# Kernel tuning notes

Hardware: AMD Instinct MI355X
Metric: run time of the kernel (lower is better)

## Reference

```python
import jax, jax.numpy as jnp
import numpy as np
from jax import lax

B, T, D = 16384, 60, 36   # n_traj, n_tp, n_dims
L, C, S = 10, 20, 9       # latent_dim, cluster_num, n_static
OUT = 8                   # mlp out (use_static=False)


def setup_inputs() -> dict:
    key = jax.random.key(0)
    ks = jax.random.split(key, 12)

    def w(k, shape):
        return jax.random.normal(k, shape, jnp.float32) / np.float32(np.sqrt(shape[0]))

    return {
        "data": jax.random.normal(ks[0], (B, T, D), jnp.float32),
        "time_steps": jnp.arange(T, dtype=jnp.float32),
        "static_data": jax.random.normal(ks[1], (B, S), jnp.float32),
        # GRU_unit_cluster gates: Linear(latent_dim + input_dim -> latent_dim)
        "W_update": w(ks[2], (L + D, L)), "b_update": jnp.zeros((L,), jnp.float32),
        "W_reset": w(ks[3], (L + D, L)), "b_reset": jnp.zeros((L,), jnp.float32),
        "W_new": w(ks[4], (L + D, L)), "b_new": jnp.zeros((L,), jnp.float32),
        # infer_emitter_z: Linear(latent_dim + cluster_num -> cluster_num)
        "W_emit": w(ks[5], (L + C, C)), "b_emit": jnp.zeros((C,), jnp.float32),
        # stand-in ODE func (z0_diffeq_solver.ode_func): tanh(Linear(latent->latent))
        "W_ode": w(ks[6], (L, L)), "b_ode": jnp.zeros((L,), jnp.float32),
        # final mlp: Linear(ts*10 + static -> 8)
        "W_mlp": w(ks[7], (T * L + S, OUT)), "b_mlp": jnp.zeros((OUT,), jnp.float32),
    }


def _forward(data, time_steps, static_data,
             W_update, b_update, W_reset, b_reset, W_new, b_new,
             W_emit, b_emit, W_ode, b_ode, W_mlp, b_mlp):
    n_traj = data.shape[0]
    # per-step dt: first step uses the synthetic 0.01 offset, then consecutive diffs
    dts = jnp.concatenate([jnp.full((1,), 0.01, time_steps.dtype), jnp.diff(time_steps)])
    xs = jnp.swapaxes(data, 0, 1)  # [T, B, D]

    def step(carry, inp):
        y_state, y_prob = carry        # [B, L], [B, C]
        x_t, dt = inp                  # [B, D], scalar
        # Euler step of the ODE between observations
        yi_ode = y_state + jnp.tanh(y_state @ W_ode + b_ode) * dt
        # GRU_unit_cluster update
        yc = jnp.concatenate([yi_ode, x_t], axis=-1)          # [B, L+D]
        u = jax.nn.sigmoid(yc @ W_update + b_update)
        r = jax.nn.sigmoid(yc @ W_reset + b_reset)
        cc = jnp.concatenate([yi_ode * r, x_t], axis=-1)
        new = cc @ W_new + b_new
        y_new = (1.0 - u) * new + u * yi_ode                  # [B, L]
        # emit_probs (concat_data=True path)
        zin = jnp.concatenate([y_prob, y_new], axis=-1)       # [B, C+L]
        y_prob_new = jax.nn.softmax(zin @ W_emit + b_emit, axis=-1)
        return (y_new, y_prob_new), y_new

    init = (jnp.zeros((n_traj, L), data.dtype), jnp.zeros((n_traj, C), data.dtype))
    _, states = lax.scan(step, init, (xs, dts))               # states: [T, B, L]

    vec = jnp.swapaxes(states, 0, 1).reshape(n_traj, T * L)   # [B, T*L]
    vec = jnp.concatenate([vec, static_data], axis=-1)        # [B, T*L + S]
    return vec @ W_mlp + b_mlp                                # [B, 8]


def reference(data, time_steps, static_data,
              W_update, b_update, W_reset, b_reset, W_new, b_new,
              W_emit, b_emit, W_ode, b_ode, W_mlp, b_mlp):
    return _forward(data, time_steps, static_data,
                    W_update, b_update, W_reset, b_reset, W_new, b_new,
                    W_emit, b_emit, W_ode, b_ode, W_mlp, b_mlp)
```

## Files before the change

kernel.cpp:

```cpp
#include <hip/hip_runtime.h>
#include <hip/hip_fp16.h>
#include <math.h>

#define B_TRAJ 16384
#define T_STEPS 60
#define D_IN 36
#define L_DIM 10
#define C_NUM 20
#define S_STAT 9
#define OUT_DIM 8
#define TT 2
#define NTILE (T_STEPS / TT)

#define LOG2E 1.4426950408889634f

typedef float f32x2 __attribute__((ext_vector_type(2)));
__device__ __forceinline__ f32x2 pkfma(f32x2 a, f32x2 b, f32x2 c) {
    return __builtin_elementwise_fma(a, b, c);
}

__device__ __forceinline__ float rcp_fast(float x) { return __builtin_amdgcn_rcpf(x); }
__device__ __forceinline__ float exp2_fast(float x) { return __builtin_amdgcn_exp2f(x); }
__device__ __forceinline__ float sigm_fast(float x) {
    return rcp_fast(1.0f + exp2_fast(x * -LOG2E));
}
__device__ __forceinline__ float tanh_fast(float x) {
    const float t = fminf(fmaxf(x * (2.0f * LOG2E), -30.0f), 30.0f);
    return fmaf(-2.0f, rcp_fast(exp2_fast(t) + 1.0f), 1.0f);
}
#define WFENCE() __builtin_amdgcn_wave_barrier()

__global__ __launch_bounds__(256) __attribute__((amdgpu_waves_per_eu(4, 8)))
void dgm2_v7(
    const float* __restrict__ data,
    const float* __restrict__ time_steps,
    const float* __restrict__ static_data,
    const float* __restrict__ W_update,
    const float* __restrict__ b_update,
    const float* __restrict__ W_reset,
    const float* __restrict__ b_reset,
    const float* __restrict__ W_new,
    const float* __restrict__ b_new,
    const float* __restrict__ W_emit,
    const float* __restrict__ b_emit,
    const float* __restrict__ W_ode,
    const float* __restrict__ b_ode,
    const float* __restrict__ W_mlp,
    const float* __restrict__ b_mlp,
    float* __restrict__ out)
{
    __shared__ __align__(16) __half xprojH[8][61][32];
    __shared__ __align__(16) float WGX[D_IN][32];
    __shared__ __align__(16) float wbuf[4][292];
    __shared__ float dts[T_STEPS];

    const int tid  = threadIdx.x;
    const int w    = tid >> 6;
    const int lane = tid & 63;
    const int half = lane >> 5;
    const int s    = lane & 31;
    const int ltraj = w * 2 + half;
    const int traj  = blockIdx.x * 8 + ltraj;

    for (int i = tid; i < D_IN * 30; i += 256) {
        const int k = i / 30, c = i % 30;
        float v;
        if (c < 10)      v = W_update[(L_DIM + k) * L_DIM + c];
        else if (c < 20) v = W_reset [(L_DIM + k) * L_DIM + (c - 10)];
        else             v = W_new   [(L_DIM + k) * L_DIM + (c - 20)];
        WGX[k][c] = v;
    }
    for (int i = tid; i < D_IN * 2; i += 256) WGX[i >> 1][30 + (i & 1)] = 0.0f;
    if (tid < T_STEPS) dts[tid] = (tid == 0) ? 0.01f : time_steps[tid] - time_steps[tid - 1];
    __syncthreads();

    float bcol = 0.0f;
    if (s < 10)      bcol = b_update[s];
    else if (s < 20) bcol = b_reset[s - 10];
    else if (s < 30) bcol = b_new[s - 20];

    {
        f32x2 wxp2[18];
#pragma unroll
        for (int j = 0; j < 18; ++j) wxp2[j] = (f32x2){WGX[2 * j][s], WGX[2 * j + 1][s]};

        float* xst = &wbuf[w][0];
        const float* tbase = data + (size_t)(blockIdx.x * 8 + w * 2) * (T_STEPS * D_IN);
        const int sh  = lane / 18;
        const int sr  = lane % 18;
        const int stt = sr / 9;
        const int sc  = sr % 9;
        const bool stg = (lane < 36);

        if (stg) {
            const float4 v = *reinterpret_cast<const float4*>(
                tbase + (size_t)sh * (T_STEPS * D_IN) + stt * D_IN + sc * 4);
            *reinterpret_cast<float4*>(xst + ((0 * 2 + sh) * TT + stt) * 36 + sc * 4) = v;
        }
        WFENCE();

        for (int tile = 0; tile < NTILE; ++tile) {
            const int cb = tile & 1, nb = cb ^ 1;
            float4 pf = make_float4(0.f, 0.f, 0.f, 0.f);
            if (stg && (tile + 1 < NTILE)) {
                pf = *reinterpret_cast<const float4*>(
                    tbase + (size_t)sh * (T_STEPS * D_IN) + ((tile + 1) * TT + stt) * D_IN + sc * 4);
            }
#pragma unroll
            for (int tt = 0; tt < TT; ++tt) {
                const float* xrow = xst + ((cb * 2 + half) * TT + tt) * 36;
                f32x2 acc2 = (f32x2){bcol, 0.0f};
#pragma unroll
                for (int c = 0; c < 9; ++c) {
                    const float4 x4 = *reinterpret_cast<const float4*>(xrow + c * 4);
                    acc2 = pkfma((f32x2){x4.x, x4.y}, wxp2[2 * c],     acc2);
                    acc2 = pkfma((f32x2){x4.z, x4.w}, wxp2[2 * c + 1], acc2);
                }
                if (s < 30) xprojH[ltraj][tile * TT + tt][s] = __float2half(acc2.x + acc2.y);
            }
            if (stg && (tile + 1 < NTILE)) {
                *reinterpret_cast<float4*>(xst + ((nb * 2 + sh) * TT + stt) * 36 + sc * 4) = pf;
            }
            WFENCE();
        }
    }

    const bool uo = (s < 10);
    const bool ro = (s >= 10 && s < 20);
    const bool no = (s >= 20 && s < 30);
    const bool eo = (s >= 10 && s < 30);
    const int  gcol = uo ? s : (ro ? (s - 10) : (no ? (s - 20) : 0));

    const float* Wg = uo ? W_update : (ro ? W_reset : W_new);
    f32x2 wgy2[5];
#pragma unroll
    for (int j = 0; j < 5; ++j) {
        const float w0 = (s < 30) ? Wg[(2 * j)     * L_DIM + gcol] : 0.0f;
        const float w1 = (s < 30) ? Wg[(2 * j + 1) * L_DIM + gcol] : 0.0f;
        wgy2[j] = (f32x2){w0, w1};
    }

    f32x2 waux2[15];
#pragma unroll
    for (int j = 0; j < 15; ++j) {
        float v0 = 0.0f, v1 = 0.0f;
        if (eo)            { v0 = W_emit[(2 * j) * C_NUM + (s - 10)];
                             v1 = W_emit[(2 * j + 1) * C_NUM + (s - 10)]; }
        else if (uo && j < 5) { v0 = W_ode[(2 * j) * L_DIM + s];
                                v1 = W_ode[(2 * j + 1) * L_DIM + s]; }
        waux2[j] = (f32x2){v0, v1};
    }
    const float bode  = uo ? b_ode[s] : 0.0f;
    const float bemit = eo ? b_emit[s - 10] : 0.0f;

    float* bcYI = &wbuf[w][0]  + half * 12;
    float* bcR  = &wbuf[w][24] + half * 12;
    float* bcN  = &wbuf[w][48] + half * 12;
    float* bcY  = &wbuf[w][72] + half * 12;
    float* bcP  = &wbuf[w][96] + half * 20;

    f32x2 y2[5];
#pragma unroll
    for (int k = 0; k < 5; ++k) y2[k] = (f32x2){0.0f, 0.0f};
    float yown = 0.0f;
    if (eo) bcP[s - 10] = 0.0f;
    WFENCE();

    for (int t = 0; t < T_STEPS; ++t) {
        const float dt = dts[t];

        f32x2 g2 = (f32x2){bode, 0.0f};
#pragma unroll
        for (int k = 0; k < 5; ++k) g2 = pkfma(y2[k], waux2[k], g2);
        const float yis = fmaf(tanh_fast(g2.x + g2.y), dt, yown);
        if (uo) bcYI[s] = yis;
        WFENCE();
        {
            const float4 a = *reinterpret_cast<const float4*>(bcYI);
            const float4 b = *reinterpret_cast<const float4*>(bcYI + 4);
            const float2 c = *reinterpret_cast<const float2*>(bcYI + 8);
            y2[0] = (f32x2){a.x, a.y}; y2[1] = (f32x2){a.z, a.w};
            y2[2] = (f32x2){b.x, b.y}; y2[3] = (f32x2){b.z, b.w};
            y2[4] = (f32x2){c.x, c.y};
        }
        const float yi_r = bcYI[gcol];

        const float xa = __half2float(xprojH[ltraj][t][s]);
        f32x2 ay2 = (f32x2){xa, 0.0f};
#pragma unroll
        for (int k = 0; k < 5; ++k) ay2 = pkfma(y2[k], wgy2[k], ay2);
        const float uval = sigm_fast(ay2.x + ay2.y);
        if (ro) bcR[s - 10] = uval * yi_r;
        WFENCE();

        f32x2 n2 = (f32x2){xa, 0.0f};
        {
            const float4 a = *reinterpret_cast<const float4*>(bcR);
            const float4 b = *reinterpret_cast<const float4*>(bcR + 4);
            const float2 c = *reinterpret_cast<const float2*>(bcR + 8);
            n2 = pkfma((f32x2){a.x, a.y}, wgy2[0], n2);
            n2 = pkfma((f32x2){a.z, a.w}, wgy2[1], n2);
            n2 = pkfma((f32x2){b.x, b.y}, wgy2[2], n2);
            n2 = pkfma((f32x2){b.z, b.w}, wgy2[3], n2);
            n2 = pkfma((f32x2){c.x, c.y}, wgy2[4], n2);
        }
        const float accN = n2.x + n2.y;
        if (no) bcN[s - 20] = accN;
        WFENCE();

        if (uo) {
            const float nv = bcN[s];
            const float yn = fmaf(uval, yis - nv, nv);
            yown = yn;
            bcY[s] = yn;
            xprojH[ltraj][t][s] = __float2half(yn);
        }
        WFENCE();
        {
            const float4 a = *reinterpret_cast<const float4*>(bcY);
            const float4 b = *reinterpret_cast<const float4*>(bcY + 4);
            const float2 c = *reinterpret_cast<const float2*>(bcY + 8);
            y2[0] = (f32x2){a.x, a.y}; y2[1] = (f32x2){a.z, a.w};
            y2[2] = (f32x2){b.x, b.y}; y2[3] = (f32x2){b.z, b.w};
            y2[4] = (f32x2){c.x, c.y};
        }

        f32x2 zd2 = (f32x2){0.0f, 0.0f};
        f32x2 zs2 = (f32x2){0.0f, 0.0f};
#pragma unroll
        for (int q = 0; q < 5; ++q) {
            const float4 z4 = *reinterpret_cast<const float4*>(bcP + q * 4);
            const f32x2 za = (f32x2){z4.x, z4.y};
            const f32x2 zb = (f32x2){z4.z, z4.w};
            zd2 = pkfma(za, waux2[2 * q],     zd2);
            zd2 = pkfma(zb, waux2[2 * q + 1], zd2);
            zs2 = zs2 + za + zb;
        }
        const float zsum = zs2.x + zs2.y;
        const float pinv = (t == 0) ? 0.0f : rcp_fast(zsum);
        f32x2 ev2 = (f32x2){fmaf(zd2.x + zd2.y, pinv, bemit), 0.0f};
#pragma unroll
        for (int k = 0; k < 5; ++k) ev2 = pkfma(y2[k], waux2[10 + k], ev2);
        const float zv = exp2_fast(fminf((ev2.x + ev2.y) * LOG2E, 86.0f));
        if (eo) bcP[s - 10] = zv;
        WFENCE();
    }

    WFENCE();
    {
        const int g = s >> 3, col = s & 7;
        f32x2 o2 = (f32x2){0.0f, 0.0f};
        for (int tb = 0; tb < 15; ++tb) {
            const int t = g + tb * 4;
            const __half2* yh = reinterpret_cast<const __half2*>(&xprojH[ltraj][t][0]);
            const float* wrow = W_mlp + (size_t)t * L_DIM * OUT_DIM + col;
#pragma unroll
            for (int q = 0; q < 5; ++q) {
                const float2 yv = __half22float2(yh[q]);
                const f32x2 w2 = (f32x2){wrow[(2 * q) * OUT_DIM], wrow[(2 * q + 1) * OUT_DIM]};
                o2 = pkfma((f32x2){yv.x, yv.y}, w2, o2);
            }
        }
        float o8 = o2.x + o2.y;
        o8 += __shfl_xor(o8, 8, 32);
        o8 += __shfl_xor(o8, 16, 32);
        if (s < OUT_DIM) {
            const float* stp = static_data + (size_t)traj * S_STAT;
            const float* wms = W_mlp + (size_t)(T_STEPS * L_DIM) * OUT_DIM;
#pragma unroll
            for (int i = 0; i < S_STAT; ++i) o8 += stp[i] * wms[i * OUT_DIM + s];
            out[(size_t)traj * OUT_DIM + s] = o8 + b_mlp[s];
        }
    }
}

extern "C" void kernel_launch(void* const* d_in, const int* in_sizes, int n_in,
                              void* d_out, int out_size, void* d_ws, size_t ws_size,
                              hipStream_t stream) {
    const float* data        = (const float*)d_in[0];
    const float* time_steps  = (const float*)d_in[1];
    const float* static_data = (const float*)d_in[2];
    const float* W_update    = (const float*)d_in[3];
    const float* b_update    = (const float*)d_in[4];
    const float* W_reset     = (const float*)d_in[5];
    const float* b_reset     = (const float*)d_in[6];
    const float* W_new       = (const float*)d_in[7];
    const float* b_new       = (const float*)d_in[8];
    const float* W_emit      = (const float*)d_in[9];
    const float* b_emit      = (const float*)d_in[10];
    const float* W_ode       = (const float*)d_in[11];
    const float* b_ode       = (const float*)d_in[12];
    const float* W_mlp       = (const float*)d_in[13];
    const float* b_mlp       = (const float*)d_in[14];
    float* out = (float*)d_out;

    dim3 grid(B_TRAJ / 8), block(256);
    hipLaunchKernelGGL(dgm2_v7, grid, block, 0, stream,
                       data, time_steps, static_data,
                       W_update, b_update, W_reset, b_reset, W_new, b_new,
                       W_emit, b_emit, W_ode, b_ode, W_mlp, b_mlp, out);
}
```

Before: 339.8 us.

## Shrink LDS footprint, drop WGX staging, and cut per-step wave barriers

Removes the shared WGX weight table and loads the input-projection weights straight from global memory into registers. The xproj buffer is packed to a stride of 30 and the staging buffer to a single slot, which shrinks LDS per block and should allow more resident blocks. The GRU combine now runs on the new-gate lanes using a broadcast update gate, which drops one LDS exchange and one barrier per step, and the trailing barrier in the step loop is also removed. In exchange the prefetch is no longer double-buffered and needs an extra barrier per tile, and dropping the end-of-step barrier relies on wave-level ordering for the bcP read/write hazard.

```diff
diff --git a/kernel.cpp b/kernel.cpp
--- a/kernel.cpp
+++ b/kernel.cpp
@@ -11,6 +11,7 @@
 #define OUT_DIM 8
 #define TT 2
 #define NTILE (T_STEPS / TT)
+#define XTS 1824
 
 #define LOG2E 1.4426950408889634f
 
@@ -31,7 +32,7 @@
 #define WFENCE() __builtin_amdgcn_wave_barrier()
 
 __global__ __launch_bounds__(256) __attribute__((amdgpu_waves_per_eu(4, 8)))
-void dgm2_v7(
+void dgm2_v8(
     const float* __restrict__ data,
     const float* __restrict__ time_steps,
     const float* __restrict__ static_data,
@@ -49,9 +50,8 @@
     const float* __restrict__ b_mlp,
     float* __restrict__ out)
 {
-    __shared__ __align__(16) __half xprojH[8][61][32];
-    __shared__ __align__(16) float WGX[D_IN][32];
-    __shared__ __align__(16) float wbuf[4][292];
+    __shared__ __align__(16) __half xprojH[8 * XTS];
+    __shared__ __align__(16) float wbuf[4][144];
     __shared__ float dts[T_STEPS];
 
     const int tid  = threadIdx.x;
@@ -61,28 +61,29 @@
     const int s    = lane & 31;
     const int ltraj = w * 2 + half;
     const int traj  = blockIdx.x * 8 + ltraj;
-
-    for (int i = tid; i < D_IN * 30; i += 256) {
-        const int k = i / 30, c = i % 30;
-        float v;
-        if (c < 10)      v = W_update[(L_DIM + k) * L_DIM + c];
-        else if (c < 20) v = W_reset [(L_DIM + k) * L_DIM + (c - 10)];
-        else             v = W_new   [(L_DIM + k) * L_DIM + (c - 20)];
-        WGX[k][c] = v;
-    }
-    for (int i = tid; i < D_IN * 2; i += 256) WGX[i >> 1][30 + (i & 1)] = 0.0f;
+    __half* xpj = xprojH + ltraj * XTS;
+
     if (tid < T_STEPS) dts[tid] = (tid == 0) ? 0.01f : time_steps[tid] - time_steps[tid - 1];
     __syncthreads();
 
+    const bool uo = (s < 10);
+    const bool ro = (s >= 10 && s < 20);
+    const bool no = (s >= 20 && s < 30);
+    const bool eo = (s >= 10 && s < 30);
+    const int  gcol = uo ? s : (ro ? (s - 10) : (no ? (s - 20) : 0));
+    const float* Wg = uo ? W_update : (ro ? W_reset : W_new);
+
     float bcol = 0.0f;
-    if (s < 10)      bcol = b_update[s];
-    else if (s < 20) bcol = b_reset[s - 10];
-    else if (s < 30) bcol = b_new[s - 20];
+    if (uo)      bcol = b_update[s];
+    else if (ro) bcol = b_reset[s - 10];
+    else if (no) bcol = b_new[s - 20];
 
     {
         f32x2 wxp2[18];
 #pragma unroll
-        for (int j = 0; j < 18; ++j) wxp2[j] = (f32x2){WGX[2 * j][s], WGX[2 * j + 1][s]};
+        for (int j = 0; j < 18; ++j)
+            wxp2[j] = (f32x2){Wg[(L_DIM + 2 * j) * L_DIM + gcol],
+                              Wg[(L_DIM + 2 * j + 1) * L_DIM + gcol]};
 
         float* xst = &wbuf[w][0];
         const float* tbase = data + (size_t)(blockIdx.x * 8 + w * 2) * (T_STEPS * D_IN);
@@ -95,20 +96,20 @@
         if (stg) {
             const float4 v = *reinterpret_cast<const float4*>(
                 tbase + (size_t)sh * (T_STEPS * D_IN) + stt * D_IN + sc * 4);
-            *reinterpret_cast<float4*>(xst + ((0 * 2 + sh) * TT + stt) * 36 + sc * 4) = v;
+            *reinterpret_cast<float4*>(xst + (sh * TT + stt) * 36 + sc * 4) = v;
         }
         WFENCE();
 
         for (int tile = 0; tile < NTILE; ++tile) {
-            const int cb = tile & 1, nb = cb ^ 1;
             float4 pf = make_float4(0.f, 0.f, 0.f, 0.f);
-            if (stg && (tile + 1 < NTILE)) {
+            const bool more = stg && (tile + 1 < NTILE);
+            if (more) {
                 pf = *reinterpret_cast<const float4*>(
                     tbase + (size_t)sh * (T_STEPS * D_IN) + ((tile + 1) * TT + stt) * D_IN + sc * 4);
             }
 #pragma unroll
             for (int tt = 0; tt < TT; ++tt) {
-                const float* xrow = xst + ((cb * 2 + half) * TT + tt) * 36;
+                const float* xrow = xst + (half * TT + tt) * 36;
                 f32x2 acc2 = (f32x2){bcol, 0.0f};
 #pragma unroll
                 for (int c = 0; c < 9; ++c) {
@@ -116,36 +117,27 @@
                     acc2 = pkfma((f32x2){x4.x, x4.y}, wxp2[2 * c],     acc2);
                     acc2 = pkfma((f32x2){x4.z, x4.w}, wxp2[2 * c + 1], acc2);
                 }
-                if (s < 30) xprojH[ltraj][tile * TT + tt][s] = __float2half(acc2.x + acc2.y);
-            }
-            if (stg && (tile + 1 < NTILE)) {
-                *reinterpret_cast<float4*>(xst + ((nb * 2 + sh) * TT + stt) * 36 + sc * 4) = pf;
+                if (s < 30) xpj[(tile * TT + tt) * 30 + s] = __float2half(acc2.x + acc2.y);
             }
             WFENCE();
-        }
-    }
-
-    const bool uo = (s < 10);
-    const bool ro = (s >= 10 && s < 20);
-    const bool no = (s >= 20 && s < 30);
-    const bool eo = (s >= 10 && s < 30);
-    const int  gcol = uo ? s : (ro ? (s - 10) : (no ? (s - 20) : 0));
-
-    const float* Wg = uo ? W_update : (ro ? W_reset : W_new);
+            if (more) {
+                *reinterpret_cast<float4*>(xst + (sh * TT + stt) * 36 + sc * 4) = pf;
+            }
+            WFENCE();
+        }
+    }
+
     f32x2 wgy2[5];
 #pragma unroll
-    for (int j = 0; j < 5; ++j) {
-        const float w0 = (s < 30) ? Wg[(2 * j)     * L_DIM + gcol] : 0.0f;
-        const float w1 = (s < 30) ? Wg[(2 * j + 1) * L_DIM + gcol] : 0.0f;
-        wgy2[j] = (f32x2){w0, w1};
-    }
+    for (int j = 0; j < 5; ++j)
+        wgy2[j] = (f32x2){Wg[(2 * j) * L_DIM + gcol], Wg[(2 * j + 1) * L_DIM + gcol]};
 
     f32x2 waux2[15];
 #pragma unroll
     for (int j = 0; j < 15; ++j) {
         float v0 = 0.0f, v1 = 0.0f;
-        if (eo)            { v0 = W_emit[(2 * j) * C_NUM + (s - 10)];
-                             v1 = W_emit[(2 * j + 1) * C_NUM + (s - 10)]; }
+        if (eo)               { v0 = W_emit[(2 * j) * C_NUM + (s - 10)];
+                                v1 = W_emit[(2 * j + 1) * C_NUM + (s - 10)]; }
         else if (uo && j < 5) { v0 = W_ode[(2 * j) * L_DIM + s];
                                 v1 = W_ode[(2 * j + 1) * L_DIM + s]; }
         waux2[j] = (f32x2){v0, v1};
@@ -153,11 +145,12 @@
     const float bode  = uo ? b_ode[s] : 0.0f;
     const float bemit = eo ? b_emit[s - 10] : 0.0f;
 
-    float* bcYI = &wbuf[w][0]  + half * 12;
-    float* bcR  = &wbuf[w][24] + half * 12;
-    float* bcN  = &wbuf[w][48] + half * 12;
-    float* bcY  = &wbuf[w][72] + half * 12;
-    float* bcP  = &wbuf[w][96] + half * 20;
+    float* wb   = &wbuf[w][0];
+    float* bcYI = wb + 0  + half * 12;
+    float* bcR  = wb + 24 + half * 12;
+    float* bcU  = wb + 48 + half * 12;
+    float* bcY  = wb + 72 + half * 12;
+    float* bcP  = wb + 96 + half * 20;
 
     f32x2 y2[5];
 #pragma unroll
@@ -183,14 +176,15 @@
             y2[2] = (f32x2){b.x, b.y}; y2[3] = (f32x2){b.z, b.w};
             y2[4] = (f32x2){c.x, c.y};
         }
-        const float yi_r = bcYI[gcol];
-
-        const float xa = __half2float(xprojH[ltraj][t][s]);
+        const float yi_g = bcYI[gcol];
+
+        const float xa = __half2float(xpj[t * 30 + s]);
         f32x2 ay2 = (f32x2){xa, 0.0f};
 #pragma unroll
         for (int k = 0; k < 5; ++k) ay2 = pkfma(y2[k], wgy2[k], ay2);
         const float uval = sigm_fast(ay2.x + ay2.y);
-        if (ro) bcR[s - 10] = uval * yi_r;
+        if (ro) bcR[s - 10] = uval * yi_g;
+        if (uo) bcU[s] = uval;
         WFENCE();
 
         f32x2 n2 = (f32x2){xa, 0.0f};
@@ -205,15 +199,11 @@
             n2 = pkfma((f32x2){c.x, c.y}, wgy2[4], n2);
         }
         const float accN = n2.x + n2.y;
-        if (no) bcN[s - 20] = accN;
-        WFENCE();
-
-        if (uo) {
-            const float nv = bcN[s];
-            const float yn = fmaf(uval, yis - nv, nv);
-            yown = yn;
-            bcY[s] = yn;
-            xprojH[ltraj][t][s] = __float2half(yn);
+        const float u_n  = bcU[gcol];
+        const float yn   = fmaf(u_n, yi_g - accN, accN);
+        if (no) {
+            bcY[s - 20] = yn;
+            xpj[t * 30 + (s - 20)] = __float2half(yn);
         }
         WFENCE();
         {
@@ -224,6 +214,7 @@
             y2[2] = (f32x2){b.x, b.y}; y2[3] = (f32x2){b.z, b.w};
             y2[4] = (f32x2){c.x, c.y};
         }
+        yown = bcY[gcol];
 
         f32x2 zd2 = (f32x2){0.0f, 0.0f};
         f32x2 zs2 = (f32x2){0.0f, 0.0f};
@@ -243,7 +234,6 @@
         for (int k = 0; k < 5; ++k) ev2 = pkfma(y2[k], waux2[10 + k], ev2);
         const float zv = exp2_fast(fminf((ev2.x + ev2.y) * LOG2E, 86.0f));
         if (eo) bcP[s - 10] = zv;
-        WFENCE();
     }
 
     WFENCE();
@@ -252,7 +242,7 @@
         f32x2 o2 = (f32x2){0.0f, 0.0f};
         for (int tb = 0; tb < 15; ++tb) {
             const int t = g + tb * 4;
-            const __half2* yh = reinterpret_cast<const __half2*>(&xprojH[ltraj][t][0]);
+            const __half2* yh = reinterpret_cast<const __half2*>(xpj + t * 30);
             const float* wrow = W_mlp + (size_t)t * L_DIM * OUT_DIM + col;
 #pragma unroll
             for (int q = 0; q < 5; ++q) {
@@ -295,7 +285,7 @@
     float* out = (float*)d_out;
 
     dim3 grid(B_TRAJ / 8), block(256);
-    hipLaunchKernelGGL(dgm2_v7, grid, block, 0, stream,
+    hipLaunchKernelGGL(dgm2_v8, grid, block, 0, stream,
                        data, time_steps, static_data,
                        W_update, b_update, W_reset, b_reset, W_new, b_new,
                        W_emit, b_emit, W_ode, b_ode, W_mlp, b_mlp, out);
```

Measured after the change: 330.6 us. -2.7%, faster.
